# Optimization experiments

Measured on AMD Instinct MI355X. Metric: run time of the kernel, lower is better.

The kernel has to match this reference:

```python
import jax, jax.numpy as jnp
import numpy as np
import math

B, L, D = 8, 2048, 256


def setup_inputs() -> dict:
    key = jax.random.key(0)
    ks = jax.random.split(key, 8)
    return {
        "query": jax.random.normal(ks[0], (B, L, D), dtype=jnp.float32),
        "key": jax.random.normal(ks[1], (B, L, D), dtype=jnp.float32),
        "value": jax.random.normal(ks[2], (B, L, D), dtype=jnp.float32),
        "mask": jax.random.randint(ks[3], (B, L), 0, 2, dtype=jnp.int32),
        "Wq_w": jax.random.normal(ks[4], (D, D), dtype=jnp.float32) * 0.05,
        "Wq_b": jax.random.normal(ks[5], (D,), dtype=jnp.float32) * 0.05,
        "Wk_w": jax.random.normal(ks[6], (D, D), dtype=jnp.float32) * 0.05,
        "Wk_b": jax.random.normal(ks[7], (D,), dtype=jnp.float32) * 0.05,
    }


def reference(query, key, value, mask, Wq_w, Wq_b, Wk_w, Wk_b):
    d = query.shape[-1]
    q = query @ Wq_w.T + Wq_b            # [B, Lq, D]
    k = key @ Wk_w.T + Wk_b              # [B, Lk, D]
    scores = jnp.einsum("bqd,bkd->bqk", q, k) / math.sqrt(d)  # [B, Lq, Lk]
    m = mask.astype(scores.dtype)[:, None, :]                  # [B, 1, Lk]
    # multiplicative then additive masking, as in original
    scores = jnp.where(m == 0, jnp.asarray(-1e9, scores.dtype), scores * m)
    attn = jax.nn.softmax(scores, axis=-1)
    return jnp.einsum("bqk,bkd->bqd", attn, value)
```

## Files before the change

### kernel.cpp

```cpp
#include <hip/hip_runtime.h>
#include <stdint.h>
#include <stddef.h>

#define B_ 8
#define L_ 2048
#define D_ 256
#define KSPLIT 4
#define KRANGE 512
#define KTILE 32
#define NITER 16
#define PSS 40

typedef __bf16 bf16x8 __attribute__((ext_vector_type(8)));
typedef float floatx4 __attribute__((ext_vector_type(4)));
typedef _Float16 half4_t __attribute__((ext_vector_type(4)));

__device__ __forceinline__ short f2bf(float f) {
    union { float f; uint32_t u; } v; v.f = f;
    uint32_t u = v.u;
    u += 0x7FFFu + ((u >> 16) & 1u);
    return (short)(u >> 16);
}

__device__ __forceinline__ uint32_t pack2bf(float a, float b) {
    union { float f; uint32_t u; } x, y; x.f = a; y.f = b;
    uint32_t ua = x.u + (0x7FFFu + ((x.u >> 16) & 1u));
    uint32_t ub = y.u + (0x7FFFu + ((y.u >> 16) & 1u));
    return (ua >> 16) | (ub & 0xFFFF0000u);
}

__device__ __forceinline__ void async16(const void* g, void* l) {
    __builtin_amdgcn_global_load_lds(
        (__attribute__((address_space(1))) void*)g,
        (__attribute__((address_space(3))) void*)l,
        16, 0, 0);
}

__global__ __launch_bounds__(256, 2) void proj_kernel(
    const float* __restrict__ Xq, const float* __restrict__ Xk,
    const float* __restrict__ Wq, const float* __restrict__ Wk,
    const float* __restrict__ bq, const float* __restrict__ bk,
    short* __restrict__ Oq, short* __restrict__ Ok)
{
    const float* X    = blockIdx.y ? Xk : Xq;
    const float* W    = blockIdx.y ? Wk : Wq;
    const float* bias = blockIdx.y ? bk : bq;
    short* Out        = blockIdx.y ? Ok : Oq;

    __shared__ uint32_t As[64 * 20];
    __shared__ uint32_t Ws[256 * 20];

    const int tid  = threadIdx.x;
    const int wid  = tid >> 6;
    const int lane = tid & 63;
    const int m16  = lane & 15;
    const int quad = lane >> 4;
    const int row0 = blockIdx.x * 64;

    floatx4 acc[16];
    const floatx4 z4 = {0.f, 0.f, 0.f, 0.f};
#pragma unroll
    for (int i = 0; i < 16; i++) acc[i] = z4;

    for (int kc = 0; kc < 8; kc++) {
        const int k0 = kc * 32;
        __syncthreads();
        {
            int r = tid >> 2, cg = tid & 3;
            const float* src = X + (size_t)(row0 + r) * D_ + k0 + cg * 8;
            float4 a = *(const float4*)src;
            float4 b2 = *(const float4*)(src + 4);
            uint4 u;
            u.x = pack2bf(a.x, a.y);  u.y = pack2bf(a.z, a.w);
            u.z = pack2bf(b2.x, b2.y); u.w = pack2bf(b2.z, b2.w);
            *(uint4*)&As[r * 20 + cg * 4] = u;
        }
#pragma unroll
        for (int p = 0; p < 4; p++) {
            int r = p * 64 + (tid >> 2), cg = tid & 3;
            const float* src = W + (size_t)r * D_ + k0 + cg * 8;
            float4 a = *(const float4*)src;
            float4 b2 = *(const float4*)(src + 4);
            uint4 u;
            u.x = pack2bf(a.x, a.y);  u.y = pack2bf(a.z, a.w);
            u.z = pack2bf(b2.x, b2.y); u.w = pack2bf(b2.z, b2.w);
            *(uint4*)&Ws[r * 20 + cg * 4] = u;
        }
        __syncthreads();
        bf16x8 af = *(const bf16x8*)&As[(wid * 16 + m16) * 20 + quad * 4];
#pragma unroll
        for (int n = 0; n < 16; n++) {
            bf16x8 bfr = *(const bf16x8*)&Ws[(n * 16 + m16) * 20 + quad * 4];
            acc[n] = __builtin_amdgcn_mfma_f32_16x16x32_bf16(af, bfr, acc[n], 0, 0, 0);
        }
    }
#pragma unroll
    for (int n = 0; n < 16; n++) {
        const int col = n * 16 + m16;
        const float bv = bias[col];
#pragma unroll
        for (int r = 0; r < 4; r++) {
            const int row = row0 + wid * 16 + quad * 4 + r;
            Out[(size_t)row * D_ + col] = f2bf(acc[n][r] + bv);
        }
    }
}

__global__ __launch_bounds__(256, 2) void vtrans_kernel(
    const float* __restrict__ V, short* __restrict__ Vt)
{
    __shared__ uint32_t T[256 * 20];
    const int tid = threadIdx.x;
    const int b  = blockIdx.y;
    const int l0 = blockIdx.x * 32;
    const int r2 = tid >> 4;
    const int dg = tid & 15;
    const int lp = r2 ^ ((dg & 3) << 2);
#pragma unroll
    for (int p = 0; p < 4; p++) {
        int d0 = (dg + p * 16) * 4;
        const float* src = V + ((size_t)b * L_ + l0 + r2 * 2) * D_ + d0;
        float4 e0 = *(const float4*)src;
        float4 e1 = *(const float4*)(src + D_);
        T[(d0 + 0) * 20 + lp] = pack2bf(e0.x, e1.x);
        T[(d0 + 1) * 20 + lp] = pack2bf(e0.y, e1.y);
        T[(d0 + 2) * 20 + lp] = pack2bf(e0.z, e1.z);
        T[(d0 + 3) * 20 + lp] = pack2bf(e0.w, e1.w);
    }
    __syncthreads();
#pragma unroll
    for (int p = 0; p < 4; p++) {
        int d = (tid >> 2) + p * 64;
        int c = tid & 3;
        int cp = c ^ ((d >> 2) & 3);
        uint4 u = *(const uint4*)&T[d * 20 + cp * 4];
        *(uint4*)(Vt + ((size_t)b * D_ + d) * L_ + l0 + c * 8) = u;
    }
}

__global__ __launch_bounds__(256, 2) void flash_kernel(
    const short* __restrict__ Qb, const short* __restrict__ Kb,
    const short* __restrict__ Vt, const int* __restrict__ mask,
    float* __restrict__ Out, _Float16* __restrict__ Part,
    float* __restrict__ Lpart)
{
    __shared__ short Ks[2][KTILE * 256];
    __shared__ short Vs[2][256 * KTILE];
    __shared__ short Ps[4 * 32 * PSS];

    const int tid  = threadIdx.x;
    const int wid  = tid >> 6;
    const int lane = tid & 63;
    const int m16  = lane & 15;
    const int quad = lane >> 4;
    const int b  = blockIdx.x;
    const int q0 = blockIdx.y * 128;
    const int z  = blockIdx.z;

    const short* kbase = Kb + ((size_t)b * L_ + z * KRANGE) * D_;
    const short* vbase = Vt + (size_t)b * D_ * L_;
    const int*   mg    = mask + b * L_ + z * KRANGE;

    bf16x8 qf[2][8];
    {
        const short* qrow = Qb + ((size_t)b * L_ + q0 + wid * 32) * D_;
#pragma unroll
        for (int s2 = 0; s2 < 2; s2++)
#pragma unroll
            for (int kk = 0; kk < 8; kk++)
                qf[s2][kk] = *(const bf16x8*)(qrow + (size_t)(s2 * 16 + m16) * D_ + kk * 32 + quad * 8);
    }

    floatx4 o[2][16];
    const floatx4 z4 = {0.f, 0.f, 0.f, 0.f};
#pragma unroll
    for (int s2 = 0; s2 < 2; s2++)
#pragma unroll
        for (int n = 0; n < 16; n++) o[s2][n] = z4;
    float rsum[2][4] = {{0.f,0.f,0.f,0.f},{0.f,0.f,0.f,0.f}};

    auto stage = [&](int t, int bufi) {
        short* kl = &Ks[bufi][0];
        short* vl = &Vs[bufi][0];
#pragma unroll
        for (int c = 0; c < 4; c++) {
            int unit = wid * 4 + c;
            int row = unit * 2 + (lane >> 5);
            int g = (lane & 31) ^ (row & 7);
            async16(kbase + (size_t)(t * KTILE + row) * D_ + g * 8, kl + unit * 512);
        }
#pragma unroll
        for (int c = 0; c < 4; c++) {
            int unit = wid * 4 + c;
            int d = unit * 16 + (lane >> 2);
            int g = (lane & 3) ^ ((lane >> 2) & 3);
            async16(vbase + (size_t)d * L_ + z * KRANGE + t * KTILE + g * 8, vl + unit * 512);
        }
    };

    stage(0, 0);
    __builtin_amdgcn_s_waitcnt(0x0F70);
    __syncthreads();

    short* ps = Ps + wid * (32 * PSS);
    const float C2 = 0.09016844f;

    for (int t = 0; t < NITER; t++) {
        const int buf = t & 1;
        if (t + 1 < NITER) stage(t + 1, buf ^ 1);
        const short* kl = &Ks[buf][0];
        const short* vl = &Vs[buf][0];

        int mv0 = mg[t * KTILE + m16];
        int mv1 = mg[t * KTILE + 16 + m16];

        floatx4 sA[2][2];
#pragma unroll
        for (int s2 = 0; s2 < 2; s2++) { sA[s2][0] = z4; sA[s2][1] = z4; }
#pragma unroll
        for (int kk = 0; kk < 8; kk++) {
#pragma unroll
            for (int j = 0; j < 2; j++) {
                int row = j * 16 + m16;
                int cidx = (kk * 4 + quad) ^ (m16 & 7);
                bf16x8 kf = *(const bf16x8*)(kl + row * 256 + cidx * 8);
                sA[0][j] = __builtin_amdgcn_mfma_f32_16x16x32_bf16(qf[0][kk], kf, sA[0][j], 0, 0, 0);
                sA[1][j] = __builtin_amdgcn_mfma_f32_16x16x32_bf16(qf[1][kk], kf, sA[1][j], 0, 0, 0);
            }
        }

#pragma unroll
        for (int s2 = 0; s2 < 2; s2++) {
#pragma unroll
            for (int j = 0; j < 2; j++) {
                const int mv = j ? mv1 : mv0;
#pragma unroll
                for (int r = 0; r < 4; r++) {
                    float x = mv ? sA[s2][j][r] * C2 : -1.0e30f;
                    float p = exp2f(x);
                    rsum[s2][r] += p;
                    ps[(s2 * 16 + quad * 4 + r) * PSS + j * 16 + m16] = f2bf(p);
                }
            }
        }
        __builtin_amdgcn_s_waitcnt(0xC07F);
        bf16x8 pf0 = *(const bf16x8*)(ps + (size_t)m16 * PSS + quad * 8);
        bf16x8 pf1 = *(const bf16x8*)(ps + (size_t)(16 + m16) * PSS + quad * 8);

#pragma unroll
        for (int n = 0; n < 16; n++) {
            int rowd = n * 16 + m16;
            int cidx = quad ^ (m16 & 3);
            bf16x8 vf = *(const bf16x8*)(vl + rowd * 32 + cidx * 8);
            o[0][n] = __builtin_amdgcn_mfma_f32_16x16x32_bf16(pf0, vf, o[0][n], 0, 0, 0);
            o[1][n] = __builtin_amdgcn_mfma_f32_16x16x32_bf16(pf1, vf, o[1][n], 0, 0, 0);
        }

        __builtin_amdgcn_s_waitcnt(0x0F70);
        __syncthreads();
    }

#pragma unroll
    for (int s2 = 0; s2 < 2; s2++)
#pragma unroll
        for (int r = 0; r < 4; r++) {
            float x = rsum[s2][r];
            x += __shfl_xor(x, 1, 16);
            x += __shfl_xor(x, 2, 16);
            x += __shfl_xor(x, 4, 16);
            x += __shfl_xor(x, 8, 16);
            rsum[s2][r] = x;
        }

    const size_t BLD = (size_t)B_ * L_ * D_;
    const size_t rowbase = (size_t)b * L_ + q0 + wid * 32;
    if (z == 0) {
        float* po = Out + rowbase * D_;
#pragma unroll
        for (int s2 = 0; s2 < 2; s2++)
#pragma unroll
            for (int n = 0; n < 16; n++)
#pragma unroll
                for (int r = 0; r < 4; r++)
                    po[(size_t)(s2 * 16 + quad * 4 + r) * D_ + n * 16 + m16] = o[s2][n][r];
    } else {
        _Float16* pp = Part + (size_t)(z - 1) * BLD + rowbase * D_;
#pragma unroll
        for (int s2 = 0; s2 < 2; s2++)
#pragma unroll
            for (int n = 0; n < 16; n++)
#pragma unroll
                for (int r = 0; r < 4; r++)
                    pp[(size_t)(s2 * 16 + quad * 4 + r) * D_ + n * 16 + m16] = (_Float16)o[s2][n][r];
    }
    if (m16 == 0) {
#pragma unroll
        for (int s2 = 0; s2 < 2; s2++)
#pragma unroll
            for (int r = 0; r < 4; r++)
                Lpart[(size_t)z * (B_ * L_) + rowbase + s2 * 16 + quad * 4 + r] = rsum[s2][r];
    }
}

__global__ __launch_bounds__(256) void norm_kernel(
    float* __restrict__ Out, const _Float16* __restrict__ Part,
    const float* __restrict__ Lpart)
{
    const int idx = blockIdx.x * 256 + threadIdx.x;
    const int row = idx >> 6;
    const int c   = (idx & 63) * 4;
    const size_t off = (size_t)row * D_ + c;
    const size_t BLD = (size_t)B_ * L_ * D_;
    float4 acc = *(float4*)(Out + off);
#pragma unroll
    for (int zz = 0; zz < 3; zz++) {
        half4_t h = *(const half4_t*)(Part + zz * BLD + off);
        acc.x += (float)h.x; acc.y += (float)h.y;
        acc.z += (float)h.z; acc.w += (float)h.w;
    }
    const int BL = B_ * L_;
    float l = Lpart[row] + Lpart[BL + row] + Lpart[2 * BL + row] + Lpart[3 * BL + row];
    float inv = 1.0f / l;
    acc.x *= inv; acc.y *= inv; acc.z *= inv; acc.w *= inv;
    *(float4*)(Out + off) = acc;
}

extern "C" void kernel_launch(void* const* d_in, const int* in_sizes, int n_in,
                              void* d_out, int out_size, void* d_ws, size_t ws_size,
                              hipStream_t stream) {
    const float* query = (const float*)d_in[0];
    const float* key   = (const float*)d_in[1];
    const float* value = (const float*)d_in[2];
    const int*   mask  = (const int*)d_in[3];
    const float* Wq_w  = (const float*)d_in[4];
    const float* Wq_b  = (const float*)d_in[5];
    const float* Wk_w  = (const float*)d_in[6];
    const float* Wk_b  = (const float*)d_in[7];
    float* out = (float*)d_out;

    const size_t BLD = (size_t)B_ * L_ * D_;
    short* qb = (short*)d_ws;
    short* kb = qb + BLD;
    short* vt = kb + BLD;
    _Float16* part = (_Float16*)(vt + BLD);
    float* lpart = (float*)(part + 3 * BLD);

    proj_kernel<<<dim3(256, 2), 256, 0, stream>>>(query, key, Wq_w, Wk_w, Wq_b, Wk_b, qb, kb);
    vtrans_kernel<<<dim3(64, 8), 256, 0, stream>>>(value, vt);
    flash_kernel<<<dim3(8, 16, 4), 256, 0, stream>>>(qb, kb, vt, mask, out, part, lpart);
    norm_kernel<<<dim3((B_ * L_ * D_ / 4) / 256), 256, 0, stream>>>(out, part, lpart);
}
```

Before: 190.8 us.

## Software-pipeline PV matmul one tile behind QK and double-buffer projection loads

The attention loop now runs the P·V MFMAs for tile t-1 after the QK^T MFMAs for tile t. K and V tiles are staged separately so the V load for the current tile overlaps compute, and the last P·V step runs after the loop. The projection kernel gets double-buffered LDS with register prefetch of the next K-chunk, a higher occupancy hint, and bf16 rounding simplified to round-half-up. The mask select is replaced by an FMA with an additive offset. These changes aim to hide LDS, global and MFMA latency and cut ALU work, at the cost of more LDS, more registers and slightly different rounding.

```diff
diff --git a/kernel.cpp b/kernel.cpp
--- a/kernel.cpp
+++ b/kernel.cpp
@@ -17,16 +17,12 @@
 
 __device__ __forceinline__ short f2bf(float f) {
     union { float f; uint32_t u; } v; v.f = f;
-    uint32_t u = v.u;
-    u += 0x7FFFu + ((u >> 16) & 1u);
-    return (short)(u >> 16);
+    return (short)((v.u + 0x8000u) >> 16);
 }
 
 __device__ __forceinline__ uint32_t pack2bf(float a, float b) {
     union { float f; uint32_t u; } x, y; x.f = a; y.f = b;
-    uint32_t ua = x.u + (0x7FFFu + ((x.u >> 16) & 1u));
-    uint32_t ub = y.u + (0x7FFFu + ((y.u >> 16) & 1u));
-    return (ua >> 16) | (ub & 0xFFFF0000u);
+    return ((x.u + 0x8000u) >> 16) | ((y.u + 0x8000u) & 0xFFFF0000u);
 }
 
 __device__ __forceinline__ void async16(const void* g, void* l) {
@@ -36,7 +32,7 @@
         16, 0, 0);
 }
 
-__global__ __launch_bounds__(256, 2) void proj_kernel(
+__global__ __launch_bounds__(256, 3) void proj_kernel(
     const float* __restrict__ Xq, const float* __restrict__ Xk,
     const float* __restrict__ Wq, const float* __restrict__ Wk,
     const float* __restrict__ bq, const float* __restrict__ bk,
@@ -47,8 +43,8 @@
     const float* bias = blockIdx.y ? bk : bq;
     short* Out        = blockIdx.y ? Ok : Oq;
 
-    __shared__ uint32_t As[64 * 20];
-    __shared__ uint32_t Ws[256 * 20];
+    __shared__ uint32_t As[2][64 * 20];
+    __shared__ uint32_t Ws[2][256 * 20];
 
     const int tid  = threadIdx.x;
     const int wid  = tid >> 6;
@@ -56,43 +52,61 @@
     const int m16  = lane & 15;
     const int quad = lane >> 4;
     const int row0 = blockIdx.x * 64;
+    const int ar = tid >> 2, cg = tid & 3;
 
     floatx4 acc[16];
     const floatx4 z4 = {0.f, 0.f, 0.f, 0.f};
 #pragma unroll
     for (int i = 0; i < 16; i++) acc[i] = z4;
 
+    {
+        const float* srcA = X + (size_t)(row0 + ar) * D_ + cg * 8;
+        float4 a = *(const float4*)srcA, b2 = *(const float4*)(srcA + 4);
+        uint4 u; u.x = pack2bf(a.x, a.y); u.y = pack2bf(a.z, a.w);
+        u.z = pack2bf(b2.x, b2.y); u.w = pack2bf(b2.z, b2.w);
+        *(uint4*)&As[0][ar * 20 + cg * 4] = u;
+#pragma unroll
+        for (int p = 0; p < 4; p++) {
+            const float* srcW = W + (size_t)(p * 64 + ar) * D_ + cg * 8;
+            float4 wa = *(const float4*)srcW, wb = *(const float4*)(srcW + 4);
+            uint4 w; w.x = pack2bf(wa.x, wa.y); w.y = pack2bf(wa.z, wa.w);
+            w.z = pack2bf(wb.x, wb.y); w.w = pack2bf(wb.z, wb.w);
+            *(uint4*)&Ws[0][(p * 64 + ar) * 20 + cg * 4] = w;
+        }
+    }
+    __syncthreads();
+
     for (int kc = 0; kc < 8; kc++) {
-        const int k0 = kc * 32;
+        const int buf = kc & 1;
+        float4 na, nb, nwa[4], nwb[4];
+        if (kc < 7) {
+            const int k1 = (kc + 1) * 32;
+            const float* srcA = X + (size_t)(row0 + ar) * D_ + k1 + cg * 8;
+            na = *(const float4*)srcA; nb = *(const float4*)(srcA + 4);
+#pragma unroll
+            for (int p = 0; p < 4; p++) {
+                const float* srcW = W + (size_t)(p * 64 + ar) * D_ + k1 + cg * 8;
+                nwa[p] = *(const float4*)srcW; nwb[p] = *(const float4*)(srcW + 4);
+            }
+        }
+        bf16x8 af = *(const bf16x8*)&As[buf][(wid * 16 + m16) * 20 + quad * 4];
+#pragma unroll
+        for (int n = 0; n < 16; n++) {
+            bf16x8 bfr = *(const bf16x8*)&Ws[buf][(n * 16 + m16) * 20 + quad * 4];
+            acc[n] = __builtin_amdgcn_mfma_f32_16x16x32_bf16(af, bfr, acc[n], 0, 0, 0);
+        }
+        if (kc < 7) {
+            uint4 u; u.x = pack2bf(na.x, na.y); u.y = pack2bf(na.z, na.w);
+            u.z = pack2bf(nb.x, nb.y); u.w = pack2bf(nb.z, nb.w);
+            *(uint4*)&As[buf ^ 1][ar * 20 + cg * 4] = u;
+#pragma unroll
+            for (int p = 0; p < 4; p++) {
+                uint4 w; w.x = pack2bf(nwa[p].x, nwa[p].y); w.y = pack2bf(nwa[p].z, nwa[p].w);
+                w.z = pack2bf(nwb[p].x, nwb[p].y); w.w = pack2bf(nwb[p].z, nwb[p].w);
+                *(uint4*)&Ws[buf ^ 1][(p * 64 + ar) * 20 + cg * 4] = w;
+            }
+        }
         __syncthreads();
-        {
-            int r = tid >> 2, cg = tid & 3;
-            const float* src = X + (size_t)(row0 + r) * D_ + k0 + cg * 8;
-            float4 a = *(const float4*)src;
-            float4 b2 = *(const float4*)(src + 4);
-            uint4 u;
-            u.x = pack2bf(a.x, a.y);  u.y = pack2bf(a.z, a.w);
-            u.z = pack2bf(b2.x, b2.y); u.w = pack2bf(b2.z, b2.w);
-            *(uint4*)&As[r * 20 + cg * 4] = u;
-        }
-#pragma unroll
-        for (int p = 0; p < 4; p++) {
-            int r = p * 64 + (tid >> 2), cg = tid & 3;
-            const float* src = W + (size_t)r * D_ + k0 + cg * 8;
-            float4 a = *(const float4*)src;
-            float4 b2 = *(const float4*)(src + 4);
-            uint4 u;
-            u.x = pack2bf(a.x, a.y);  u.y = pack2bf(a.z, a.w);
-            u.z = pack2bf(b2.x, b2.y); u.w = pack2bf(b2.z, b2.w);
-            *(uint4*)&Ws[r * 20 + cg * 4] = u;
-        }
-        __syncthreads();
-        bf16x8 af = *(const bf16x8*)&As[(wid * 16 + m16) * 20 + quad * 4];
-#pragma unroll
-        for (int n = 0; n < 16; n++) {
-            bf16x8 bfr = *(const bf16x8*)&Ws[(n * 16 + m16) * 20 + quad * 4];
-            acc[n] = __builtin_amdgcn_mfma_f32_16x16x32_bf16(af, bfr, acc[n], 0, 0, 0);
-        }
     }
 #pragma unroll
     for (int n = 0; n < 16; n++) {
@@ -179,9 +193,8 @@
         for (int n = 0; n < 16; n++) o[s2][n] = z4;
     float rsum[2][4] = {{0.f,0.f,0.f,0.f},{0.f,0.f,0.f,0.f}};
 
-    auto stage = [&](int t, int bufi) {
+    auto stageK = [&](int t, int bufi) {
         short* kl = &Ks[bufi][0];
-        short* vl = &Vs[bufi][0];
 #pragma unroll
         for (int c = 0; c < 4; c++) {
             int unit = wid * 4 + c;
@@ -189,6 +202,9 @@
             int g = (lane & 31) ^ (row & 7);
             async16(kbase + (size_t)(t * KTILE + row) * D_ + g * 8, kl + unit * 512);
         }
+    };
+    auto stageV = [&](int t, int bufi) {
+        short* vl = &Vs[bufi][0];
 #pragma unroll
         for (int c = 0; c < 4; c++) {
             int unit = wid * 4 + c;
@@ -198,18 +214,19 @@
         }
     };
 
-    stage(0, 0);
+    stageK(0, 0);
     __builtin_amdgcn_s_waitcnt(0x0F70);
     __syncthreads();
 
     short* ps = Ps + wid * (32 * PSS);
     const float C2 = 0.09016844f;
+    bf16x8 pf0, pf1;
 
     for (int t = 0; t < NITER; t++) {
         const int buf = t & 1;
-        if (t + 1 < NITER) stage(t + 1, buf ^ 1);
+        if (t + 1 < NITER) stageK(t + 1, buf ^ 1);
+        stageV(t, buf);
         const short* kl = &Ks[buf][0];
-        const short* vl = &Vs[buf][0];
 
         int mv0 = mg[t * KTILE + m16];
         int mv1 = mg[t * KTILE + 16 + m16];
@@ -229,24 +246,43 @@
             }
         }
 
+        if (t > 0) {
+            const short* vl = &Vs[buf ^ 1][0];
+#pragma unroll
+            for (int n = 0; n < 16; n++) {
+                int rowd = n * 16 + m16;
+                int cidx = quad ^ (m16 & 3);
+                bf16x8 vf = *(const bf16x8*)(vl + rowd * 32 + cidx * 8);
+                o[0][n] = __builtin_amdgcn_mfma_f32_16x16x32_bf16(pf0, vf, o[0][n], 0, 0, 0);
+                o[1][n] = __builtin_amdgcn_mfma_f32_16x16x32_bf16(pf1, vf, o[1][n], 0, 0, 0);
+            }
+        }
+
+        float moff0 = mv0 ? 0.f : -1.0e30f;
+        float moff1 = mv1 ? 0.f : -1.0e30f;
 #pragma unroll
         for (int s2 = 0; s2 < 2; s2++) {
 #pragma unroll
             for (int j = 0; j < 2; j++) {
-                const int mv = j ? mv1 : mv0;
+                const float moff = j ? moff1 : moff0;
 #pragma unroll
                 for (int r = 0; r < 4; r++) {
-                    float x = mv ? sA[s2][j][r] * C2 : -1.0e30f;
-                    float p = exp2f(x);
+                    float p = exp2f(fmaf(sA[s2][j][r], C2, moff));
                     rsum[s2][r] += p;
                     ps[(s2 * 16 + quad * 4 + r) * PSS + j * 16 + m16] = f2bf(p);
                 }
             }
         }
         __builtin_amdgcn_s_waitcnt(0xC07F);
-        bf16x8 pf0 = *(const bf16x8*)(ps + (size_t)m16 * PSS + quad * 8);
-        bf16x8 pf1 = *(const bf16x8*)(ps + (size_t)(16 + m16) * PSS + quad * 8);
-
+        pf0 = *(const bf16x8*)(ps + (size_t)m16 * PSS + quad * 8);
+        pf1 = *(const bf16x8*)(ps + (size_t)(16 + m16) * PSS + quad * 8);
+
+        __builtin_amdgcn_s_waitcnt(0x0F70);
+        __syncthreads();
+    }
+
+    {
+        const short* vl = &Vs[(NITER - 1) & 1][0];
 #pragma unroll
         for (int n = 0; n < 16; n++) {
             int rowd = n * 16 + m16;
@@ -255,9 +291,6 @@
             o[0][n] = __builtin_amdgcn_mfma_f32_16x16x32_bf16(pf0, vf, o[0][n], 0, 0, 0);
             o[1][n] = __builtin_amdgcn_mfma_f32_16x16x32_bf16(pf1, vf, o[1][n], 0, 0, 0);
         }
-
-        __builtin_amdgcn_s_waitcnt(0x0F70);
-        __syncthreads();
     }
 
 #pragma unroll
```

After: 188.9 us. No clear change (-1.0%).
